# Kernel tuning notes

Measured on AMD Instinct MI355X. Metric: run time of the kernel, lower is better.

Reference implementation:

```python
import jax, jax.numpy as jnp
import numpy as np

B = 4          # number of graphs in the batch
M = 8192       # nodes per graph (after pooling)
N = B * M      # total pooled nodes
N0 = 2 * N     # pre-pooling node count (perm indexes into this)
D = 2          # spatial dim (2D cell coordinates)
START_K = 16
K_INCREMENT = 0


def setup_inputs() -> dict:
    key = jax.random.key(0)
    ks = jax.random.split(key, 6)
    x = jax.random.normal(ks[0], (N, 64), dtype=jnp.float32)
    pos = jax.random.uniform(ks[1], (N0, D), dtype=jnp.float32) * 1000.0
    edge_index = jax.random.randint(ks[2], (2, 1000), 0, N0, dtype=jnp.int64)
    edge_weight = jax.random.uniform(ks[3], (1000,), dtype=jnp.float32)
    batch = jnp.repeat(jnp.arange(B, dtype=jnp.int64), M)  # sorted graph ids
    perm = jax.random.randint(ks[4], (N,), 0, N0, dtype=jnp.int64)
    score = jax.random.uniform(ks[5], (N,), dtype=jnp.float32)
    return {"x": x, "pos": pos, "edge_index": edge_index,
            "edge_weight": edge_weight, "batch": batch, "perm": perm,
            "score": score, "i": 0}


def reference(x, pos, edge_index, edge_weight, batch, perm, score, i):
    k = START_K + K_INCREMENT * i
    pos_p = pos[perm]                      # [N, D] pooled positions
    posb = pos_p.reshape(B, M, D)          # batch assumed contiguous/sorted

    def knn_one(p):  # p: [M, D]
        d2 = jnp.sum((p[:, None, :] - p[None, :, :]) ** 2, axis=-1)  # [M, M]
        neg_d2, idx = jax.lax.top_k(-d2, k)  # loop=True: self (d2=0) included
        return idx, -neg_d2

    idx, d2k = jax.vmap(knn_one)(posb)      # [B, M, k]
    offs = (jnp.arange(B, dtype=idx.dtype) * M)[:, None, None]
    src = (idx + offs).reshape(-1)                         # neighbor (source)
    tgt = jnp.repeat(jnp.arange(N, dtype=src.dtype), k)    # target node
    new_edge_index = jnp.stack([src, tgt])                 # [2, N*k]

    # Distance(cat=False, norm=True): edge_attr = ||pos[row]-pos[col]|| / max
    dist = jnp.sqrt(jnp.maximum(d2k, 0.0)).reshape(-1)
    new_edge_weight = dist / jnp.max(dist)

    return (x, pos_p, new_edge_index, new_edge_weight, batch, perm, score)
```

## Files before the change

kernel.cpp:

```cpp
#include <hip/hip_runtime.h>

constexpr int B_ = 4;
constexpr int M_ = 8192;
constexpr int N_ = B_ * M_;
constexpr int K_ = 16;
constexpr int NX_ = N_ * 64;
constexpr int G_ = 16;
constexpr int C_ = G_ * G_;
constexpr int CT_ = B_ * C_;
constexpr float CW_ = 62.5f;
constexpr float INVW_ = 0.016f;
constexpr int CAP_ = 96;
constexpr int STMAX_ = 9 * CAP_;

constexpr long long OFF_X      = 0;
constexpr long long OFF_POS    = OFF_X + NX_;
constexpr long long OFF_EI_SRC = OFF_POS + 2LL * N_;
constexpr long long OFF_EI_TGT = OFF_EI_SRC + 1LL * N_ * K_;
constexpr long long OFF_W      = OFF_EI_TGT + 1LL * N_ * K_;
constexpr long long OFF_BATCH  = OFF_W + 1LL * N_ * K_;
constexpr long long OFF_PERM   = OFF_BATCH + N_;
constexpr long long OFF_SCORE  = OFF_PERM + N_;

constexpr size_t WS_COUNTS  = 0;
constexpr size_t WS_MAXBITS = 4096;
constexpr size_t WS_BPOS    = 8192;
constexpr size_t WS_BQ      = WS_BPOS + 8ull * CT_ * CAP_;

#define INSERT16(L, keyv)                                   \
  {                                                         \
    unsigned long long _k = (keyv);                         \
    _Pragma("unroll")                                       \
    for (int _t = 0; _t < K_; ++_t) {                       \
      const unsigned long long _a = (L)[_t];                \
      const bool _lt = _k < _a;                             \
      (L)[_t] = _lt ? _k : _a;                              \
      _k = _lt ? _a : _k;                                   \
    }                                                       \
  }

#define MERGE_ROUND(CUR, STRIDE)                                          \
  {                                                                       \
    unsigned long long _tmp[K_];                                          \
    _Pragma("unroll")                                                     \
    for (int _s = 0; _s < K_; ++_s) {                                     \
      const unsigned long long _pv = __shfl_xor((CUR)[K_ - 1 - _s], STRIDE, 64); \
      _tmp[_s] = (CUR)[_s] < _pv ? (CUR)[_s] : _pv;                       \
    }                                                                     \
    _Pragma("unroll")                                                     \
    for (int _k = 8; _k; _k >>= 1) {                                      \
      _Pragma("unroll")                                                   \
      for (int _i = 0; _i < K_; ++_i) {                                   \
        if ((_i & _k) == 0) {                                             \
          const unsigned long long _a = _tmp[_i], _b = _tmp[_i | _k];     \
          _tmp[_i] = _a < _b ? _a : _b;                                   \
          _tmp[_i | _k] = _a < _b ? _b : _a;                              \
        }                                                                 \
      }                                                                   \
    }                                                                     \
    _Pragma("unroll")                                                     \
    for (int _s = 0; _s < K_; ++_s) (CUR)[_s] = _tmp[_s];                 \
  }

__global__ __launch_bounds__(256) void prep_kernel(
    const float* __restrict__ x, const float* __restrict__ pos,
    const int* __restrict__ batch, const int* __restrict__ perm,
    const float* __restrict__ score, float* __restrict__ out,
    float2* __restrict__ bpos, int* __restrict__ bq,
    int* __restrict__ counts) {
  const int i = blockIdx.x * 256 + threadIdx.x;
  reinterpret_cast<float4*>(out + OFF_X)[i] =
      reinterpret_cast<const float4*>(x)[i];
  out[OFF_EI_TGT + i] = (float)(i >> 4);
  if (i < N_) {
    const int p = perm[i];
    const float px = pos[2 * p], py = pos[2 * p + 1];
    out[OFF_POS + 2 * i]     = px;
    out[OFF_POS + 2 * i + 1] = py;
    out[OFF_BATCH + i] = (float)batch[i];
    out[OFF_PERM + i]  = (float)p;
    out[OFF_SCORE + i] = score[i];
    int cx = (int)(px * INVW_); cx = cx < 0 ? 0 : (cx > 15 ? 15 : cx);
    int cy = (int)(py * INVW_); cy = cy < 0 ? 0 : (cy > 15 ? 15 : cy);
    const int cell = (i >> 13) * C_ + (cy << 4) + cx;
    const int r = atomicAdd(&counts[cell], 1);
    if (r < CAP_) {
      bpos[cell * CAP_ + r] = make_float2(px, py);
      bq[cell * CAP_ + r] = i;
    }
  }
}

__global__ __launch_bounds__(256) void knn_kernel(
    const int* __restrict__ counts, const float2* __restrict__ bpos,
    const int* __restrict__ bq, float* __restrict__ out,
    unsigned int* __restrict__ maxbits) {
  __shared__ float2 s_pos[STMAX_];
  __shared__ int    s_li[STMAX_];
  __shared__ int    s_c0[9], s_cnt[9], s_off[9];
  __shared__ int    s_tot;

  const int t = threadIdx.x;
  const int cell = blockIdx.x;
  const int qn = min(counts[cell], CAP_);
  if (qn == 0) return;

  const int g = cell >> 8;
  const int lc = cell & 255;
  const int qcx = lc & 15, qcy = lc >> 4;
  const int cb = g << 8;

  const int nx0 = qcx > 0 ? qcx - 1 : 0, nx1 = qcx < 15 ? qcx + 1 : 15;
  const int ny0 = qcy > 0 ? qcy - 1 : 0, ny1 = qcy < 15 ? qcy + 1 : 15;
  const int nw = nx1 - nx0 + 1;
  const int ncl = nw * (ny1 - ny0 + 1);
  if (t < ncl) {
    const int c = cb + ((ny0 + t / nw) << 4) + (nx0 + t % nw);
    s_c0[t] = c * CAP_;
    s_cnt[t] = min(counts[c], CAP_);
  }
  __syncthreads();
  if (t == 0) {
    int tot = 0;
    for (int r = 0; r < ncl; ++r) { s_off[r] = tot; tot += s_cnt[r]; }
    s_tot = tot;
  }
  __syncthreads();
  for (int r = 0; r < ncl; ++r) {
    const int o = s_off[r], n = s_cnt[r], c0 = s_c0[r];
    for (int j = t; j < n; j += 256) {
      s_pos[o + j] = bpos[c0 + j];
      s_li[o + j] = bq[c0 + j] & (M_ - 1);
    }
  }
  __syncthreads();

  const int tot = s_tot;
  const int rq = (qcy - ny0) * nw + (qcx - nx0);
  const int qoff = s_off[rq];
  const int qbase = cell * CAP_;
  const int grp = t >> 3, ln = t & 7;
  float mx = 0.f;

  for (int qi = grp; qi < qn; qi += 32) {
    const float2 qp = s_pos[qoff + qi];
    const float qx = qp.x, qy = qp.y;

    unsigned long long lst[K_];
#pragma unroll
    for (int s = 0; s < K_; ++s) lst[s] = ~0ull;

    int j = ln;
    for (; j + 8 < tot; j += 16) {
      const float2 c0 = s_pos[j];
      const float2 c1 = s_pos[j + 8];
      const int li0 = s_li[j], li1 = s_li[j + 8];
      const float dx0 = __fsub_rn(c0.x, qx), dy0 = __fsub_rn(c0.y, qy);
      const float d20 = __fadd_rn(__fmul_rn(dx0, dx0), __fmul_rn(dy0, dy0));
      const float dx1 = __fsub_rn(c1.x, qx), dy1 = __fsub_rn(c1.y, qy);
      const float d21 = __fadd_rn(__fmul_rn(dx1, dx1), __fmul_rn(dy1, dy1));
      const unsigned long long k0 =
          ((unsigned long long)__float_as_uint(d20) << 32) | (unsigned)li0;
      const unsigned long long k1 =
          ((unsigned long long)__float_as_uint(d21) << 32) | (unsigned)li1;
      if (k0 < lst[K_ - 1]) INSERT16(lst, k0);
      if (k1 < lst[K_ - 1]) INSERT16(lst, k1);
    }
    for (; j < tot; j += 8) {
      const float2 c0 = s_pos[j];
      const float dx = __fsub_rn(c0.x, qx), dy = __fsub_rn(c0.y, qy);
      const float d2 = __fadd_rn(__fmul_rn(dx, dx), __fmul_rn(dy, dy));
      const unsigned long long k0 =
          ((unsigned long long)__float_as_uint(d2) << 32) | (unsigned)s_li[j];
      if (k0 < lst[K_ - 1]) INSERT16(lst, k0);
    }

    MERGE_ROUND(lst, 1)
    MERGE_ROUND(lst, 2)
    MERGE_ROUND(lst, 4)

    if (ln == 0) {
      for (int c = 2; c <= 15; ++c) {
        if (lst[K_ - 1] != ~0ull) {
          const float bnd = (float)(c - 1) * CW_ - 0.01f;
          const float kth = __uint_as_float((unsigned)(lst[K_ - 1] >> 32));
          if (bnd * bnd > kth) break;
        }
        const int x0 = qcx - c, x1 = qcx + c, y0 = qcy - c, y1 = qcy + c;
        const int xs = x0 < 0 ? 0 : x0, xe = x1 > 15 ? 15 : x1;
        const int ys = y0 < 0 ? 0 : y0, ye = y1 > 15 ? 15 : y1;
        for (int y = ys; y <= ye; ++y) {
          const bool fullrow = (y == y0 || y == y1);
          for (int xx = xs; xx <= xe; ++xx) {
            if (!fullrow && xx != x0 && xx != x1) continue;
            const int cc = cb + (y << 4) + xx;
            const int s0 = cc * CAP_, e0 = s0 + min(counts[cc], CAP_);
            for (int jj = s0; jj < e0; ++jj) {
              const float2 bp = bpos[jj];
              const float dx = __fsub_rn(bp.x, qx), dy = __fsub_rn(bp.y, qy);
              const float d2 = __fadd_rn(__fmul_rn(dx, dx), __fmul_rn(dy, dy));
              const unsigned long long key =
                  ((unsigned long long)__float_as_uint(d2) << 32) |
                  (unsigned)(bq[jj] & (M_ - 1));
              if (key < lst[K_ - 1]) INSERT16(lst, key);
            }
          }
        }
      }
      const int gq = bq[qbase + qi];
      const int base = g << 13;
#pragma unroll
      for (int s = 0; s < K_; ++s) {
        const unsigned jn = (unsigned)(lst[s] & 0xffffffffu);
        const float d2 = __uint_as_float((unsigned)(lst[s] >> 32));
        const float d = sqrtf(d2);
        out[OFF_EI_SRC + (long long)gq * K_ + s] = (float)(base + (int)jn);
        out[OFF_W + (long long)gq * K_ + s] = d;
        mx = fmaxf(mx, d);
      }
    }
  }

#pragma unroll
  for (int o = 32; o; o >>= 1) mx = fmaxf(mx, __shfl_xor(mx, o, 64));
  if ((t & 63) == 0) atomicMax(maxbits, __float_as_uint(mx));
}

__global__ __launch_bounds__(256) void norm_kernel(
    float* __restrict__ out, const unsigned int* __restrict__ maxbits) {
  const float m = __uint_as_float(*maxbits);
  const int i = blockIdx.x * 256 + threadIdx.x;
  float4* w4 = reinterpret_cast<float4*>(out + OFF_W);
  float4 v = w4[i];
  v.x /= m; v.y /= m; v.z /= m; v.w /= m;
  w4[i] = v;
}

extern "C" void kernel_launch(void* const* d_in, const int* in_sizes, int n_in,
                              void* d_out, int out_size, void* d_ws, size_t ws_size,
                              hipStream_t stream) {
  const float* x     = (const float*)d_in[0];
  const float* pos   = (const float*)d_in[1];
  const int*   batch = (const int*)d_in[4];
  const int*   perm  = (const int*)d_in[5];
  const float* score = (const float*)d_in[6];
  float* out = (float*)d_out;

  char* ws = (char*)d_ws;
  int*          counts  = (int*)(ws + WS_COUNTS);
  unsigned int* maxbits = (unsigned int*)(ws + WS_MAXBITS);
  float2*       bpos    = (float2*)(ws + WS_BPOS);
  int*          bq      = (int*)(ws + WS_BQ);

  hipMemsetAsync(ws, 0, WS_MAXBITS + sizeof(unsigned int), stream);

  hipLaunchKernelGGL(prep_kernel, dim3(NX_ / 4 / 256), dim3(256), 0, stream,
                     x, pos, batch, perm, score, out, bpos, bq, counts);
  hipLaunchKernelGGL(knn_kernel, dim3(CT_), dim3(256), 0, stream,
                     counts, bpos, bq, out, maxbits);
  hipLaunchKernelGGL(norm_kernel, dim3(N_ * K_ / 4 / 256), dim3(256), 0,
                     stream, out, maxbits);
}
```

Measured before the change: 184.9 us.

## Prefilter kNN candidates with adaptive distance threshold before top-16 insertion

Before the per-lane top-16 insertion, each query estimates an upper bound from distances to same-cell points. It then counts candidates under halved, quartered and eighthed versions of that bound and picks the tightest one that still keeps at least 16 points. Only candidates under that threshold are pushed to a small per-thread LDS stack and inserted, with a full-scan fallback on overflow. This cuts expensive INSERT16 calls at the cost of two or three extra distance passes and extra LDS. The ring-search loop also skips building the key when the distance alone exceeds the current kth.

```diff
diff --git a/kernel.cpp b/kernel.cpp
--- a/kernel.cpp
+++ b/kernel.cpp
@@ -1,4 +1,5 @@
 #include <hip/hip_runtime.h>
+#include <cfloat>
 
 constexpr int B_ = 4;
 constexpr int M_ = 8192;
@@ -12,6 +13,8 @@
 constexpr float INVW_ = 0.016f;
 constexpr int CAP_ = 96;
 constexpr int STMAX_ = 9 * CAP_;
+constexpr int SCAP_ = 13;
+constexpr int SDEPTH_ = 12;
 
 constexpr long long OFF_X      = 0;
 constexpr long long OFF_POS    = OFF_X + NX_;
@@ -61,6 +64,10 @@
     _Pragma("unroll")                                                     \
     for (int _s = 0; _s < K_; ++_s) (CUR)[_s] = _tmp[_s];                 \
   }
+
+#define D2(cpx, cpy)                                                      \
+  __fadd_rn(__fmul_rn(__fsub_rn(cpx, qx), __fsub_rn(cpx, qx)),            \
+            __fmul_rn(__fsub_rn(cpy, qy), __fsub_rn(cpy, qy)))
 
 __global__ __launch_bounds__(256) void prep_kernel(
     const float* __restrict__ x, const float* __restrict__ pos,
@@ -97,6 +104,7 @@
     unsigned int* __restrict__ maxbits) {
   __shared__ float2 s_pos[STMAX_];
   __shared__ int    s_li[STMAX_];
+  __shared__ unsigned long long s_stk[256 * SCAP_];
   __shared__ int    s_c0[9], s_cnt[9], s_off[9];
   __shared__ int    s_tot;
 
@@ -140,39 +148,75 @@
   const int qoff = s_off[rq];
   const int qbase = cell * CAP_;
   const int grp = t >> 3, ln = t & 7;
+  unsigned long long* stk = &s_stk[t * SCAP_];
   float mx = 0.f;
 
   for (int qi = grp; qi < qn; qi += 32) {
     const float2 qp = s_pos[qoff + qi];
     const float qx = qp.x, qy = qp.y;
 
+    float md = 0.f;
+#pragma unroll
+    for (int m = ln; m < 16; m += 8) {
+      const int mm = m < qn ? m : 0;
+      const float2 cp = s_pos[qoff + mm];
+      const float d2p = D2(cp.x, cp.y);
+      if (m < qn) md = fmaxf(md, d2p);
+    }
+    md = fmaxf(md, __shfl_xor(md, 1, 64));
+    md = fmaxf(md, __shfl_xor(md, 2, 64));
+    md = fmaxf(md, __shfl_xor(md, 4, 64));
+    const float t0 = (qn >= K_) ? md : FLT_MAX;
+    const float t1 = t0 * 0.5f, t2 = t0 * 0.25f, t3 = t0 * 0.125f;
+
+    int pk = 0;
+    for (int j = ln; j < tot; j += 8) {
+      const float2 cp = s_pos[j];
+      const float d2 = D2(cp.x, cp.y);
+      pk += (int)(d2 <= t1) + ((int)(d2 <= t2) << 10) + ((int)(d2 <= t3) << 20);
+    }
+    pk += __shfl_xor(pk, 1, 64);
+    pk += __shfl_xor(pk, 2, 64);
+    pk += __shfl_xor(pk, 4, 64);
+    const int c1 = pk & 1023, c2 = (pk >> 10) & 1023, c3 = pk >> 20;
+    const float tau = (c3 >= K_) ? t3 : (c2 >= K_) ? t2 : (c1 >= K_) ? t1 : t0;
+
+    int sp = 0, ovf = 0;
+    for (int j = ln; j < tot; j += 8) {
+      const float2 cp = s_pos[j];
+      const float d2 = D2(cp.x, cp.y);
+      if (d2 <= tau) {
+        if (sp < SDEPTH_)
+          stk[sp++] = ((unsigned long long)__float_as_uint(d2) << 32) |
+                      (unsigned)s_li[j];
+        else
+          ovf = 1;
+      }
+    }
+    ovf |= __shfl_xor(ovf, 1, 64);
+    ovf |= __shfl_xor(ovf, 2, 64);
+    ovf |= __shfl_xor(ovf, 4, 64);
+
     unsigned long long lst[K_];
 #pragma unroll
     for (int s = 0; s < K_; ++s) lst[s] = ~0ull;
 
-    int j = ln;
-    for (; j + 8 < tot; j += 16) {
-      const float2 c0 = s_pos[j];
-      const float2 c1 = s_pos[j + 8];
-      const int li0 = s_li[j], li1 = s_li[j + 8];
-      const float dx0 = __fsub_rn(c0.x, qx), dy0 = __fsub_rn(c0.y, qy);
-      const float d20 = __fadd_rn(__fmul_rn(dx0, dx0), __fmul_rn(dy0, dy0));
-      const float dx1 = __fsub_rn(c1.x, qx), dy1 = __fsub_rn(c1.y, qy);
-      const float d21 = __fadd_rn(__fmul_rn(dx1, dx1), __fmul_rn(dy1, dy1));
-      const unsigned long long k0 =
-          ((unsigned long long)__float_as_uint(d20) << 32) | (unsigned)li0;
-      const unsigned long long k1 =
-          ((unsigned long long)__float_as_uint(d21) << 32) | (unsigned)li1;
-      if (k0 < lst[K_ - 1]) INSERT16(lst, k0);
-      if (k1 < lst[K_ - 1]) INSERT16(lst, k1);
-    }
-    for (; j < tot; j += 8) {
-      const float2 c0 = s_pos[j];
-      const float dx = __fsub_rn(c0.x, qx), dy = __fsub_rn(c0.y, qy);
-      const float d2 = __fadd_rn(__fmul_rn(dx, dx), __fmul_rn(dy, dy));
-      const unsigned long long k0 =
-          ((unsigned long long)__float_as_uint(d2) << 32) | (unsigned)s_li[j];
-      if (k0 < lst[K_ - 1]) INSERT16(lst, k0);
+    if (!ovf) {
+      for (int m = 0; m < sp; ++m) {
+        const unsigned long long k2 = stk[m];
+        if (k2 < lst[K_ - 1]) INSERT16(lst, k2);
+      }
+    } else {
+      for (int j = ln; j < tot; j += 8) {
+        const float2 cp = s_pos[j];
+        const float d2 = D2(cp.x, cp.y);
+        const unsigned db = __float_as_uint(d2);
+        if (db <= (unsigned)(lst[K_ - 1] >> 32)) {
+          const unsigned long long key =
+              ((unsigned long long)db << 32) | (unsigned)s_li[j];
+          if (key < lst[K_ - 1]) INSERT16(lst, key);
+        }
+      }
     }
 
     MERGE_ROUND(lst, 1)
@@ -197,12 +241,14 @@
             const int s0 = cc * CAP_, e0 = s0 + min(counts[cc], CAP_);
             for (int jj = s0; jj < e0; ++jj) {
               const float2 bp = bpos[jj];
-              const float dx = __fsub_rn(bp.x, qx), dy = __fsub_rn(bp.y, qy);
-              const float d2 = __fadd_rn(__fmul_rn(dx, dx), __fmul_rn(dy, dy));
-              const unsigned long long key =
-                  ((unsigned long long)__float_as_uint(d2) << 32) |
-                  (unsigned)(bq[jj] & (M_ - 1));
-              if (key < lst[K_ - 1]) INSERT16(lst, key);
+              const float d2 = D2(bp.x, bp.y);
+              const unsigned db = __float_as_uint(d2);
+              if (db <= (unsigned)(lst[K_ - 1] >> 32)) {
+                const unsigned long long key =
+                    ((unsigned long long)db << 32) |
+                    (unsigned)(bq[jj] & (M_ - 1));
+                if (key < lst[K_ - 1]) INSERT16(lst, key);
+              }
             }
           }
         }
```

New measurement: 167.2 us. 9.6% less time.
